# Kernel tuning notes

Hardware: AMD Instinct MI355X
Metric: run time of the kernel (lower is better)

Reference implementation:

```python
import jax, jax.numpy as jnp
import numpy as np

DIM_QK = 64
SCALE = DIM_QK ** 0.5


def setup_inputs() -> dict:
    key = jax.random.key(0)
    kq, kk, kv, kx = jax.random.split(key, 4)
    B, H, N, D = 4, 16, 2048, 64
    Q = jax.random.normal(kq, (B, H, N, D), dtype=jnp.float32)
    K = jax.random.normal(kk, (B, H, N, D), dtype=jnp.float32)
    V = jax.random.normal(kv, (B, H, N, D), dtype=jnp.float32)
    x = jax.random.uniform(kx, (B, 1, N, 1), dtype=jnp.float32)
    return {"Q": Q, "K": K, "V": V, "x": x}


def reference(Q, K, V, x):
    # scores: [B,H,N,N] = Q K^T / sqrt(d_k)  (no softmax)
    scores = jnp.einsum("bhnd,bhmd->bhnm", Q, K) / jnp.asarray(SCALE, Q.dtype)
    # dropout(p=0.0) is identity
    V_scaled = V * x  # broadcast [B,1,N,1] over heads/features
    out = jnp.einsum("bhnm,bhmd->bhnd", scores, V_scaled)
    return out
```

## Files before the change

kernel.cpp:

```cpp
#include <hip/hip_runtime.h>


#define BH 64
#define NROWS 2048
#define DIM 64

__global__ __launch_bounds__(256) void popattn_kv(
    const float* __restrict__ K, const float* __restrict__ V,
    const float* __restrict__ x, float* __restrict__ partial, int nchunk) {
  const int ch = blockIdx.x;
  const int bh = blockIdx.y;
  const int rows = NROWS / nchunk;
  const int m0base = ch * rows;
  const float* Kp = K + (size_t)bh * (NROWS * DIM);
  const float* Vp = V + (size_t)bh * (NROWS * DIM);
  const float* xp = x + (size_t)(bh >> 4) * NROWS;

  __shared__ float sK[32][DIM];
  __shared__ float sV[32][DIM];

  const int t = threadIdx.x;
  const int lr = t >> 4;
  const int lc = (t & 15) << 2;
  const int ti = (t >> 4) << 2;
  const int tj = (t & 15) << 2;

  float acc[4][4];
#pragma unroll
  for (int i = 0; i < 4; ++i)
#pragma unroll
    for (int j = 0; j < 4; ++j) acc[i][j] = 0.f;

  for (int m0 = m0base; m0 < m0base + rows; m0 += 32) {
    const float4 kv0 = *(const float4*)(Kp + (size_t)(m0 + lr) * DIM + lc);
    const float4 kv1 = *(const float4*)(Kp + (size_t)(m0 + 16 + lr) * DIM + lc);
    const float4 vv0 = *(const float4*)(Vp + (size_t)(m0 + lr) * DIM + lc);
    const float4 vv1 = *(const float4*)(Vp + (size_t)(m0 + 16 + lr) * DIM + lc);
    const float xv0 = xp[m0 + lr];
    const float xv1 = xp[m0 + 16 + lr];
    __syncthreads();
    *(float4*)&sK[lr][lc] = kv0;
    *(float4*)&sK[lr + 16][lc] = kv1;
    float4 vs;
    vs.x = vv0.x * xv0; vs.y = vv0.y * xv0; vs.z = vv0.z * xv0; vs.w = vv0.w * xv0;
    *(float4*)&sV[lr][lc] = vs;
    vs.x = vv1.x * xv1; vs.y = vv1.y * xv1; vs.z = vv1.z * xv1; vs.w = vv1.w * xv1;
    *(float4*)&sV[lr + 16][lc] = vs;
    __syncthreads();
#pragma unroll
    for (int mm = 0; mm < 32; ++mm) {
      const float4 ka = *(const float4*)&sK[mm][ti];
      const float4 va = *(const float4*)&sV[mm][tj];
      const float kk[4] = {ka.x, ka.y, ka.z, ka.w};
      const float vw[4] = {va.x, va.y, va.z, va.w};
#pragma unroll
      for (int ii = 0; ii < 4; ++ii)
#pragma unroll
        for (int jj = 0; jj < 4; ++jj) acc[ii][jj] += kk[ii] * vw[jj];
    }
  }

  float* Pp = partial + ((size_t)bh * nchunk + ch) * (DIM * DIM);
#pragma unroll
  for (int ii = 0; ii < 4; ++ii) {
    float4 o;
    o.x = acc[ii][0]; o.y = acc[ii][1]; o.z = acc[ii][2]; o.w = acc[ii][3];
    *(float4*)(Pp + (size_t)(ti + ii) * DIM + tj) = o;
  }
}

__global__ __launch_bounds__(256) void popattn_red(
    const float* __restrict__ partial, float* __restrict__ M, int nchunk) {
  const int e = blockIdx.x;
  const int bh = blockIdx.y;
  const int off = e * 1024 + threadIdx.x * 4;
  const float* Pp = partial + (size_t)bh * nchunk * (DIM * DIM);
  float sx = 0.f, sy = 0.f, sz = 0.f, sw = 0.f;
#pragma unroll 4
  for (int c = 0; c < nchunk; ++c) {
    const float4 p = *(const float4*)(Pp + (size_t)c * (DIM * DIM) + off);
    sx += p.x; sy += p.y; sz += p.z; sw += p.w;
  }
  float4 o;
  o.x = sx * 0.125f; o.y = sy * 0.125f; o.z = sz * 0.125f; o.w = sw * 0.125f;
  *(float4*)(M + (size_t)bh * (DIM * DIM) + off) = o;
}

__global__ __launch_bounds__(256) void popattn_qm(
    const float* __restrict__ Q, const float* __restrict__ M,
    float* __restrict__ out) {
  const int ch = blockIdx.x;
  const int bh = blockIdx.y;
  const int row0 = ch * 64;
  const float* Qp = Q + (size_t)bh * (NROWS * DIM) + (size_t)row0 * DIM;
  float* Op = out + (size_t)bh * (NROWS * DIM) + (size_t)row0 * DIM;

  __shared__ float sM[DIM * DIM];

  const int t = threadIdx.x;
  {
    const float* Mp = M + (size_t)bh * (DIM * DIM);
#pragma unroll
    for (int i = 0; i < 4; ++i) {
      const int off = i * 1024 + t * 4;
      *(float4*)&sM[off] = *(const float4*)(Mp + off);
    }
  }
  __syncthreads();

  const int r0 = t >> 3;
  const int c4 = (t & 7) * 4;

  float a00 = 0.f, a01 = 0.f, a02 = 0.f, a03 = 0.f;
  float a04 = 0.f, a05 = 0.f, a06 = 0.f, a07 = 0.f;
  float a10 = 0.f, a11 = 0.f, a12 = 0.f, a13 = 0.f;
  float a14 = 0.f, a15 = 0.f, a16 = 0.f, a17 = 0.f;

#pragma unroll
  for (int kg = 0; kg < 16; ++kg) {
    const float4 qa = *(const float4*)(Qp + (size_t)r0 * DIM + kg * 4);
    const float4 qb = *(const float4*)(Qp + (size_t)(r0 + 32) * DIM + kg * 4);
    const float qav[4] = {qa.x, qa.y, qa.z, qa.w};
    const float qbv[4] = {qb.x, qb.y, qb.z, qb.w};
#pragma unroll
    for (int dk = 0; dk < 4; ++dk) {
      const int k = kg * 4 + dk;
      const float4 m0 = *(const float4*)&sM[k * DIM + c4];
      const float4 m1 = *(const float4*)&sM[k * DIM + c4 + 32];
      const float q0 = qav[dk], q1 = qbv[dk];
      a00 += q0 * m0.x; a01 += q0 * m0.y; a02 += q0 * m0.z; a03 += q0 * m0.w;
      a04 += q0 * m1.x; a05 += q0 * m1.y; a06 += q0 * m1.z; a07 += q0 * m1.w;
      a10 += q1 * m0.x; a11 += q1 * m0.y; a12 += q1 * m0.z; a13 += q1 * m0.w;
      a14 += q1 * m1.x; a15 += q1 * m1.y; a16 += q1 * m1.z; a17 += q1 * m1.w;
    }
  }

  float4 o;
  o.x = a00; o.y = a01; o.z = a02; o.w = a03;
  *(float4*)(Op + (size_t)r0 * DIM + c4) = o;
  o.x = a04; o.y = a05; o.z = a06; o.w = a07;
  *(float4*)(Op + (size_t)r0 * DIM + c4 + 32) = o;
  o.x = a10; o.y = a11; o.z = a12; o.w = a13;
  *(float4*)(Op + (size_t)(r0 + 32) * DIM + c4) = o;
  o.x = a14; o.y = a15; o.z = a16; o.w = a17;
  *(float4*)(Op + (size_t)(r0 + 32) * DIM + c4 + 32) = o;
}

extern "C" void kernel_launch(void* const* d_in, const int* in_sizes, int n_in,
                              void* d_out, int out_size, void* d_ws, size_t ws_size,
                              hipStream_t stream) {
  const float* Q = (const float*)d_in[0];
  const float* K = (const float*)d_in[1];
  const float* V = (const float*)d_in[2];
  const float* x = (const float*)d_in[3];
  float* out = (float*)d_out;
  float* partial = (float*)d_ws;

  int nchunk = 16;
  while (nchunk > 1 &&
         ((size_t)BH * nchunk * DIM * DIM + (size_t)BH * DIM * DIM) * sizeof(float) > ws_size)
    nchunk >>= 1;
  float* Mbuf = partial + (size_t)BH * nchunk * DIM * DIM;

  dim3 blk(256);
  popattn_kv<<<dim3(nchunk, BH), blk, 0, stream>>>(K, V, x, partial, nchunk);
  popattn_red<<<dim3(4, BH), blk, 0, stream>>>(partial, Mbuf, nchunk);
  popattn_qm<<<dim3(NROWS / 64, BH), blk, 0, stream>>>(Q, Mbuf, out);
}
```

Measured before the change: 44.23 us.

## Use 8x8 register tiles with in-block wave reduction and larger QM row blocks

The K^T·V kernel now gives each wave a quarter of the 32-row tile and each thread an 8x8 output block, which cuts shared-memory loads per FMA. The four waves' partial sums are then combined through shared memory in serialized steps before one store per block. The Q·M kernel processes 256 rows per block with an 8x8 register tile per thread, reusing each sM load across 8 rows. Costs: 64+ accumulator registers may lower occupancy, the QM grid shrinks to 8 blocks per head, and the in-block reduction adds extra barriers.

```diff
diff --git a/kernel.cpp b/kernel.cpp
--- a/kernel.cpp
+++ b/kernel.cpp
@@ -16,20 +16,23 @@
   const float* Vp = V + (size_t)bh * (NROWS * DIM);
   const float* xp = x + (size_t)(bh >> 4) * NROWS;
 
-  __shared__ float sK[32][DIM];
-  __shared__ float sV[32][DIM];
+  __shared__ float smem[4096];
+  float (*sK)[DIM] = (float(*)[DIM])smem;
+  float (*sV)[DIM] = (float(*)[DIM])(smem + 2048);
 
   const int t = threadIdx.x;
   const int lr = t >> 4;
   const int lc = (t & 15) << 2;
-  const int ti = (t >> 4) << 2;
-  const int tj = (t & 15) << 2;
-
-  float acc[4][4];
-#pragma unroll
-  for (int i = 0; i < 4; ++i)
-#pragma unroll
-    for (int j = 0; j < 4; ++j) acc[i][j] = 0.f;
+  const int wv = t >> 6;
+  const int l = t & 63;
+  const int ti = (l >> 3) << 3;
+  const int tj = (l & 7) << 3;
+
+  float acc[8][8];
+#pragma unroll
+  for (int i = 0; i < 8; ++i)
+#pragma unroll
+    for (int j = 0; j < 8; ++j) acc[i][j] = 0.f;
 
   for (int m0 = m0base; m0 < m0base + rows; m0 += 32) {
     const float4 kv0 = *(const float4*)(Kp + (size_t)(m0 + lr) * DIM + lc);
@@ -48,24 +51,52 @@
     *(float4*)&sV[lr + 16][lc] = vs;
     __syncthreads();
 #pragma unroll
-    for (int mm = 0; mm < 32; ++mm) {
-      const float4 ka = *(const float4*)&sK[mm][ti];
-      const float4 va = *(const float4*)&sV[mm][tj];
-      const float kk[4] = {ka.x, ka.y, ka.z, ka.w};
-      const float vw[4] = {va.x, va.y, va.z, va.w};
-#pragma unroll
-      for (int ii = 0; ii < 4; ++ii)
-#pragma unroll
-        for (int jj = 0; jj < 4; ++jj) acc[ii][jj] += kk[ii] * vw[jj];
-    }
+    for (int mm = 0; mm < 8; ++mm) {
+      const int row = wv * 8 + mm;
+      const float4 ka0 = *(const float4*)&sK[row][ti];
+      const float4 ka1 = *(const float4*)&sK[row][ti + 4];
+      const float4 vb0 = *(const float4*)&sV[row][tj];
+      const float4 vb1 = *(const float4*)&sV[row][tj + 4];
+      const float kk[8] = {ka0.x, ka0.y, ka0.z, ka0.w, ka1.x, ka1.y, ka1.z, ka1.w};
+      const float vw[8] = {vb0.x, vb0.y, vb0.z, vb0.w, vb1.x, vb1.y, vb1.z, vb1.w};
+#pragma unroll
+      for (int ii = 0; ii < 8; ++ii)
+#pragma unroll
+        for (int jj = 0; jj < 8; ++jj) acc[ii][jj] += kk[ii] * vw[jj];
+    }
+  }
+
+  __syncthreads();
+#pragma unroll 1
+  for (int s2 = 0; s2 < 4; ++s2) {
+    if (wv == s2) {
+#pragma unroll
+      for (int ii = 0; ii < 8; ++ii) {
+        float* dst = &smem[(ti + ii) * DIM + tj];
+        if (s2 == 0) {
+          float4 o;
+          o.x = acc[ii][0]; o.y = acc[ii][1]; o.z = acc[ii][2]; o.w = acc[ii][3];
+          *(float4*)dst = o;
+          o.x = acc[ii][4]; o.y = acc[ii][5]; o.z = acc[ii][6]; o.w = acc[ii][7];
+          *(float4*)(dst + 4) = o;
+        } else {
+          float4 a = *(float4*)dst;
+          a.x += acc[ii][0]; a.y += acc[ii][1]; a.z += acc[ii][2]; a.w += acc[ii][3];
+          *(float4*)dst = a;
+          a = *(float4*)(dst + 4);
+          a.x += acc[ii][4]; a.y += acc[ii][5]; a.z += acc[ii][6]; a.w += acc[ii][7];
+          *(float4*)(dst + 4) = a;
+        }
+      }
+    }
+    __syncthreads();
   }
 
   float* Pp = partial + ((size_t)bh * nchunk + ch) * (DIM * DIM);
 #pragma unroll
-  for (int ii = 0; ii < 4; ++ii) {
-    float4 o;
-    o.x = acc[ii][0]; o.y = acc[ii][1]; o.z = acc[ii][2]; o.w = acc[ii][3];
-    *(float4*)(Pp + (size_t)(ti + ii) * DIM + tj) = o;
+  for (int i = 0; i < 4; ++i) {
+    const int idx = (t + 256 * i) * 4;
+    *(float4*)(Pp + idx) = *(const float4*)&smem[idx];
   }
 }
 
@@ -91,7 +122,7 @@
     float* __restrict__ out) {
   const int ch = blockIdx.x;
   const int bh = blockIdx.y;
-  const int row0 = ch * 64;
+  const int row0 = ch * 256;
   const float* Qp = Q + (size_t)bh * (NROWS * DIM) + (size_t)row0 * DIM;
   float* Op = out + (size_t)bh * (NROWS * DIM) + (size_t)row0 * DIM;
 
@@ -108,42 +139,45 @@
   }
   __syncthreads();
 
-  const int r0 = t >> 3;
-  const int c4 = (t & 7) * 4;
-
-  float a00 = 0.f, a01 = 0.f, a02 = 0.f, a03 = 0.f;
-  float a04 = 0.f, a05 = 0.f, a06 = 0.f, a07 = 0.f;
-  float a10 = 0.f, a11 = 0.f, a12 = 0.f, a13 = 0.f;
-  float a14 = 0.f, a15 = 0.f, a16 = 0.f, a17 = 0.f;
-
-#pragma unroll
+  const int r = t >> 3;
+  const int c8 = (t & 7) * 8;
+
+  float acc[8][8];
+#pragma unroll
+  for (int rr = 0; rr < 8; ++rr)
+#pragma unroll
+    for (int jj = 0; jj < 8; ++jj) acc[rr][jj] = 0.f;
+
+#pragma unroll 2
   for (int kg = 0; kg < 16; ++kg) {
-    const float4 qa = *(const float4*)(Qp + (size_t)r0 * DIM + kg * 4);
-    const float4 qb = *(const float4*)(Qp + (size_t)(r0 + 32) * DIM + kg * 4);
-    const float qav[4] = {qa.x, qa.y, qa.z, qa.w};
-    const float qbv[4] = {qb.x, qb.y, qb.z, qb.w};
+    float4 qv[8];
+#pragma unroll
+    for (int rr = 0; rr < 8; ++rr)
+      qv[rr] = *(const float4*)(Qp + (size_t)(r + 32 * rr) * DIM + kg * 4);
 #pragma unroll
     for (int dk = 0; dk < 4; ++dk) {
       const int k = kg * 4 + dk;
-      const float4 m0 = *(const float4*)&sM[k * DIM + c4];
-      const float4 m1 = *(const float4*)&sM[k * DIM + c4 + 32];
-      const float q0 = qav[dk], q1 = qbv[dk];
-      a00 += q0 * m0.x; a01 += q0 * m0.y; a02 += q0 * m0.z; a03 += q0 * m0.w;
-      a04 += q0 * m1.x; a05 += q0 * m1.y; a06 += q0 * m1.z; a07 += q0 * m1.w;
-      a10 += q1 * m0.x; a11 += q1 * m0.y; a12 += q1 * m0.z; a13 += q1 * m0.w;
-      a14 += q1 * m1.x; a15 += q1 * m1.y; a16 += q1 * m1.z; a17 += q1 * m1.w;
-    }
-  }
-
-  float4 o;
-  o.x = a00; o.y = a01; o.z = a02; o.w = a03;
-  *(float4*)(Op + (size_t)r0 * DIM + c4) = o;
-  o.x = a04; o.y = a05; o.z = a06; o.w = a07;
-  *(float4*)(Op + (size_t)r0 * DIM + c4 + 32) = o;
-  o.x = a10; o.y = a11; o.z = a12; o.w = a13;
-  *(float4*)(Op + (size_t)(r0 + 32) * DIM + c4) = o;
-  o.x = a14; o.y = a15; o.z = a16; o.w = a17;
-  *(float4*)(Op + (size_t)(r0 + 32) * DIM + c4 + 32) = o;
+      const float4 m0 = *(const float4*)&sM[k * DIM + c8];
+      const float4 m1 = *(const float4*)&sM[k * DIM + c8 + 4];
+      const float mm[8] = {m0.x, m0.y, m0.z, m0.w, m1.x, m1.y, m1.z, m1.w};
+#pragma unroll
+      for (int rr = 0; rr < 8; ++rr) {
+        const float q = (dk == 0) ? qv[rr].x : (dk == 1) ? qv[rr].y
+                       : (dk == 2) ? qv[rr].z : qv[rr].w;
+#pragma unroll
+        for (int jj = 0; jj < 8; ++jj) acc[rr][jj] += q * mm[jj];
+      }
+    }
+  }
+
+#pragma unroll
+  for (int rr = 0; rr < 8; ++rr) {
+    float4 o;
+    o.x = acc[rr][0]; o.y = acc[rr][1]; o.z = acc[rr][2]; o.w = acc[rr][3];
+    *(float4*)(Op + (size_t)(r + 32 * rr) * DIM + c8) = o;
+    o.x = acc[rr][4]; o.y = acc[rr][5]; o.z = acc[rr][6]; o.w = acc[rr][7];
+    *(float4*)(Op + (size_t)(r + 32 * rr) * DIM + c8 + 4) = o;
+  }
 }
 
 extern "C" void kernel_launch(void* const* d_in, const int* in_sizes, int n_in,
@@ -165,5 +199,5 @@
   dim3 blk(256);
   popattn_kv<<<dim3(nchunk, BH), blk, 0, stream>>>(K, V, x, partial, nchunk);
   popattn_red<<<dim3(4, BH), blk, 0, stream>>>(partial, Mbuf, nchunk);
-  popattn_qm<<<dim3(NROWS / 64, BH), blk, 0, stream>>>(Q, Mbuf, out);
-}
+  popattn_qm<<<dim3(NROWS / 256, BH), blk, 0, stream>>>(Q, Mbuf, out);
+}
```

New measurement: 53.57 us. 21.1% more time.
